# Performance work log

Measured on AMD Instinct MI355X. Metric: run time of the kernel, lower is better.

The kernel has to match this reference:

```python
import jax, jax.numpy as jnp
import numpy as np

B, LATENT = 8192, 1024
NR, NC = 12, 12                      # nb_rows, nb_cols
H0, W0 = NR + 2, NC + 2              # 14x14 after reshape
EPS = 1e-5
SLOPE = 0.01                         # LeakyReLU default


def setup_inputs() -> dict:
    key = jax.random.key(0)
    ks = jax.random.split(key, 9)
    s = 0.05
    return {
        "x": jax.random.normal(ks[0], (B, LATENT), jnp.float32),
        "fc_w": jax.random.normal(ks[1], (H0 * W0 * 36, LATENT), jnp.float32) * s,
        "fc_b": jax.random.normal(ks[2], (H0 * W0 * 36,), jnp.float32) * s,
        "conv_w": jax.random.normal(ks[3], (16, 36, 2, 2), jnp.float32) * s,
        "conv_b": jax.random.normal(ks[4], (16,), jnp.float32) * s,
        "gamma": jnp.ones((16,), jnp.float32),
        "beta": jnp.zeros((16,), jnp.float32),
        # locally-connected weights: (out_ch, in_ch, Hout, Wout, k*k)
        "lw1": jax.random.normal(ks[5], (6, 16, H0 - 1, W0 - 1, 4), jnp.float32) * s,
        "lw2": jax.random.normal(ks[6], (1, 6, H0 - 2, W0 - 2, 4), jnp.float32) * s,
    }


def _leaky(x):
    return jnp.where(x >= 0, x, SLOPE * x)


def _local_conv2(x, w):
    # x: (B,C,H,W); w: (O,C,Ho,Wo,4) with k=2, stride 1, no padding
    Ho, Wo = w.shape[2], w.shape[3]
    patches = jnp.stack(
        [x[:, :, dy:dy + Ho, dx:dx + Wo] for dy in (0, 1) for dx in (0, 1)],
        axis=-1)  # (B,C,Ho,Wo,4)
    return jnp.einsum('bchwk,ochwk->bohw', patches, w)


def reference(x, fc_w, fc_b, conv_w, conv_b, gamma, beta, lw1, lw2):
    # fc -> view(B, H0, W0, 36) -> permute to NCHW
    h = x @ fc_w.T + fc_b
    h = h.reshape(B, H0, W0, 36).transpose(0, 3, 1, 2)  # (B,36,14,14)
    # Conv2d k=2 padding='same' (torch pads bottom/right for even kernels)
    h = jax.lax.conv_general_dilated(
        h, conv_w, window_strides=(1, 1), padding=((0, 1), (0, 1)),
        dimension_numbers=('NCHW', 'OIHW', 'NCHW')) + conv_b[None, :, None, None]
    h = _leaky(h)
    # BatchNorm2d (training mode: batch stats, biased var)
    mu = h.mean(axis=(0, 2, 3), keepdims=True)
    var = h.var(axis=(0, 2, 3), keepdims=True)
    h = (h - mu) * jax.lax.rsqrt(var + EPS)
    h = h * gamma[None, :, None, None] + beta[None, :, None, None]
    # locally-connected stack: 14x14 -> 13x13 -> 12x12
    h = _leaky(_local_conv2(h, lw1))
    return _local_conv2(h, lw2)  # (B,1,12,12)
```

## Files before the change

kernel.cpp:

```cpp
#include <hip/hip_runtime.h>


#define SLOPE 0.01f

typedef __bf16 bf16x8 __attribute__((ext_vector_type(8)));
typedef float f32x4 __attribute__((ext_vector_type(4)));

typedef const __attribute__((address_space(1))) void* gas_ptr;
typedef __attribute__((address_space(3))) void* las_ptr;

__device__ __forceinline__ void load16_to_lds(const void* g, void* l) {
  __builtin_amdgcn_global_load_lds((gas_ptr)g, (las_ptr)l, 16, 0, 0);
}

__device__ __forceinline__ unsigned short f2bf(float f) {
  union { float f; unsigned int u; } v; v.f = f;
  unsigned int r = v.u + 0x7FFFu + ((v.u >> 16) & 1u);
  return (unsigned short)(r >> 16);
}
__device__ __forceinline__ float bfbits2f(unsigned int bits16) {
  union { unsigned int u; float f; } v; v.u = bits16 << 16;
  return v.f;
}
__device__ __forceinline__ float leaky(float v) { return v >= 0.f ? v : SLOPE * v; }

__global__ void k_cast_x(const float* __restrict__ x, unsigned short* __restrict__ xb,
                         float* __restrict__ stats) {
  if (blockIdx.x == 0 && threadIdx.x < 32) stats[threadIdx.x] = 0.f;
  int gid = blockIdx.x * 256 + threadIdx.x;
  const float4* x4 = (const float4*)x;
  float4 a = x4[gid * 2], b = x4[gid * 2 + 1];
  union { unsigned short s[8]; uint4 v; } o;
  o.s[0] = f2bf(a.x); o.s[1] = f2bf(a.y); o.s[2] = f2bf(a.z); o.s[3] = f2bf(a.w);
  o.s[4] = f2bf(b.x); o.s[5] = f2bf(b.y); o.s[6] = f2bf(b.z); o.s[7] = f2bf(b.w);
  ((uint4*)xb)[gid] = o.v;
}

__global__ void k_fold(const float* __restrict__ fc_w, const float* __restrict__ fc_b,
                       const float* __restrict__ conv_w, const float* __restrict__ conv_b,
                       unsigned short* __restrict__ Wc, float* __restrict__ bc) {
  __shared__ float cw[2304];
  int blk = blockIdx.x, kg = blockIdx.y, t = threadIdx.x;
  if (blk == 196) {
    if (kg != 0) return;
    uint4 z = make_uint4(0, 0, 0, 0);
    uint4* dst = (uint4*)(Wc + 3136 * 1024);
    for (int i = t; i < 8192; i += 256) dst[i] = z;
    for (int i = 3136 + t; i < 3200; i += 256) bc[i] = 0.f;
    return;
  }
  for (int i = t; i < 2304; i += 256) cw[i] = conv_w[i];
  __syncthreads();
  int i0 = blk / 14, j0 = blk - (blk / 14) * 14;
  int kcol = kg * 256 + t;
  float acc[16];
#pragma unroll
  for (int o = 0; o < 16; o++) acc[o] = 0.f;
  for (int c = 0; c < 36; c++) {
#pragma unroll
    for (int dy = 0; dy < 2; dy++) {
      int ii = i0 + dy; if (ii > 13) continue;
#pragma unroll
      for (int dx = 0; dx < 2; dx++) {
        int jj = j0 + dx; if (jj > 13) continue;
        int row = (ii * 14 + jj) * 36 + c;
        float f = fc_w[row * 1024 + kcol];
        int kk = dy * 2 + dx;
#pragma unroll
        for (int o = 0; o < 16; o++)
          acc[o] += cw[(o * 36 + c) * 4 + kk] * f;
      }
    }
  }
#pragma unroll
  for (int o = 0; o < 16; o++) {
    int n = o * 196 + i0 * 14 + j0;
    Wc[n * 1024 + kcol] = f2bf(acc[o]);
  }
  if (kg == 0 && t < 16) {
    int o = t;
    float b = conv_b[o];
    for (int c = 0; c < 36; c++)
      for (int dy = 0; dy < 2; dy++) {
        int ii = i0 + dy; if (ii > 13) continue;
        for (int dx = 0; dx < 2; dx++) {
          int jj = j0 + dx; if (jj > 13) continue;
          b += cw[(o * 36 + c) * 4 + dy * 2 + dx] * fc_b[(ii * 14 + jj) * 36 + c];
        }
      }
    bc[o * 196 + i0 * 14 + j0] = b;
  }
}

__global__ __launch_bounds__(256, 4) void k_gemm(const unsigned short* __restrict__ Xb,
                                                 const unsigned short* __restrict__ Wcb,
                                                 const float* __restrict__ bc,
                                                 unsigned short* __restrict__ h2,
                                                 float* __restrict__ stats) {
  __shared__ __align__(16) char lds[32768];
  __shared__ float red[4][4];
  const int t = threadIdx.x;
  const int w = t >> 6, lane = t & 63;
  const int quad = lane >> 4, l15 = lane & 15;
  const int bid = blockIdx.x;
  const int xcd = bid & 7, j = bid >> 3;
  const int mblk = xcd * 8 + (j & 7);
  const int nblk = j >> 3;
  const int m0 = mblk * 128, n0 = nblk * 128;
  const int mrow = t & 127, tko = t >> 7;
  const unsigned short* ga = Xb + (m0 + mrow) * 1024 + tko * 8;
  const unsigned short* gb = Wcb + (n0 + mrow) * 1024 + tko * 8;
  char* lA = lds;
  char* lB = lds + 16384;
  const int wbase = w * 1024;
  const int wm0 = (w >> 1) * 64, wn0 = (w & 1) * 64;

  f32x4 acc[4][4];
#pragma unroll
  for (int a = 0; a < 4; a++)
#pragma unroll
    for (int b = 0; b < 4; b++) acc[a][b] = (f32x4){0.f, 0.f, 0.f, 0.f};

  for (int kb = 0; kb < 1024; kb += 64) {
    __syncthreads();
#pragma unroll
    for (int i = 0; i < 4; i++) {
      load16_to_lds(ga + kb + i * 16, lA + i * 4096 + wbase);
      load16_to_lds(gb + kb + i * 16, lB + i * 4096 + wbase);
    }
    __syncthreads();

#pragma unroll
    for (int kk = 0; kk < 2; kk++) {
      bf16x8 af[4], bfr[4];
#pragma unroll
      for (int mb = 0; mb < 4; mb++)
        af[mb] = *(const bf16x8*)(lA + (kk * 4 + quad) * 2048 + (wm0 + mb * 16 + l15) * 16);
#pragma unroll
      for (int nb = 0; nb < 4; nb++)
        bfr[nb] = *(const bf16x8*)(lB + (kk * 4 + quad) * 2048 + (wn0 + nb * 16 + l15) * 16);
#pragma unroll
      for (int mb = 0; mb < 4; mb++)
#pragma unroll
        for (int nb = 0; nb < 4; nb++)
          acc[mb][nb] = __builtin_amdgcn_mfma_f32_16x16x32_bf16(af[mb], bfr[nb], acc[mb][nb], 0, 0, 0);
    }
  }

  const int cLo = n0 / 196;
  const int cHi = (n0 + 127) / 196;
  float ss0 = 0.f, ss1 = 0.f, sq0 = 0.f, sq1 = 0.f;
#pragma unroll
  for (int nb = 0; nb < 4; nb++) {
    int col = n0 + wn0 + nb * 16 + l15;
    float bias = bc[col];
    int ch = col / 196;
    bool hi = (ch != cLo);
    bool valid = col < 3136;
    float cs = 0.f, cq = 0.f;
#pragma unroll
    for (int mb = 0; mb < 4; mb++) {
#pragma unroll
      for (int r = 0; r < 4; r++) {
        int row = m0 + wm0 + mb * 16 + quad * 4 + r;
        float v = leaky(acc[mb][nb][r] + bias);
        h2[row * 3200 + col] = f2bf(v);
        cs += v; cq += v * v;
      }
    }
    if (valid) {
      if (hi) { ss1 += cs; sq1 += cq; } else { ss0 += cs; sq0 += cq; }
    }
  }
#pragma unroll
  for (int off = 1; off < 64; off <<= 1) {
    ss0 += __shfl_xor(ss0, off, 64);
    ss1 += __shfl_xor(ss1, off, 64);
    sq0 += __shfl_xor(sq0, off, 64);
    sq1 += __shfl_xor(sq1, off, 64);
  }
  if (lane == 0) { red[w][0] = ss0; red[w][1] = ss1; red[w][2] = sq0; red[w][3] = sq1; }
  __syncthreads();
  if (t == 0) {
    float a0 = red[0][0] + red[1][0] + red[2][0] + red[3][0];
    float a1 = red[0][1] + red[1][1] + red[2][1] + red[3][1];
    float b0 = red[0][2] + red[1][2] + red[2][2] + red[3][2];
    float b1 = red[0][3] + red[1][3] + red[2][3] + red[3][3];
    atomicAdd(&stats[cLo], a0);
    atomicAdd(&stats[16 + cLo], b0);
    if (cHi != cLo && cHi < 16) {
      atomicAdd(&stats[cHi], a1);
      atomicAdd(&stats[16 + cHi], b1);
    }
  }
}

__global__ __launch_bounds__(256) void k_tail(const unsigned short* __restrict__ h2,
                                              const float* __restrict__ stats,
                                              const float* __restrict__ gamma,
                                              const float* __restrict__ beta,
                                              const float* __restrict__ lw1,
                                              const float* __restrict__ lw2,
                                              float* __restrict__ out) {
  __shared__ unsigned short h3[4 * 3138];
  __shared__ float h4[4 * 1015];
  __shared__ float sc[16], sh[16];
  int b0 = blockIdx.x * 4, t = threadIdx.x;
  if (t < 16) {
    const float inv = 1.f / 1605632.f;
    float mean = stats[t] * inv;
    float var = stats[16 + t] * inv - mean * mean;
    float rstd = rsqrtf(var + 1e-5f);
    float s = gamma[t] * rstd;
    sc[t] = s; sh[t] = beta[t] - mean * s;
  }
  __syncthreads();
  for (int i = t; i < 6272; i += 256) {
    int bb = i / 1568, q = i - bb * 1568;
    int n = q * 2, o = n / 196;
    unsigned int u = *(const unsigned int*)(h2 + (b0 + bb) * 3200 + n);
    float v0 = bfbits2f(u & 0xffffu) * sc[o] + sh[o];
    float v1 = bfbits2f(u >> 16) * sc[o] + sh[o];
    unsigned int pk = (unsigned int)f2bf(v0) | ((unsigned int)f2bf(v1) << 16);
    *(unsigned int*)(h3 + bb * 3138 + n) = pk;
  }
  __syncthreads();
  for (int u = t; u < 312; u += 256) {
    int bb = u & 3, rest = u >> 2;
    int o = rest / 13, y = rest - o * 13;
    float acc[13];
#pragma unroll
    for (int x = 0; x < 13; x++) acc[x] = 0.f;
    const unsigned short* hb = h3 + bb * 3138;
    for (int c = 0; c < 16; c++) {
      float r0[14], r1[14];
      const unsigned int* p0 = (const unsigned int*)(hb + c * 196 + y * 14);
      const unsigned int* p1 = (const unsigned int*)(hb + c * 196 + (y + 1) * 14);
#pragma unroll
      for (int q = 0; q < 7; q++) {
        unsigned int v0 = p0[q], v1 = p1[q];
        r0[2 * q] = bfbits2f(v0 & 0xffffu); r0[2 * q + 1] = bfbits2f(v0 >> 16);
        r1[2 * q] = bfbits2f(v1 & 0xffffu); r1[2 * q + 1] = bfbits2f(v1 >> 16);
      }
      const float4* wp4 = (const float4*)(lw1 + (((o * 16 + c) * 13 + y) * 13) * 4);
#pragma unroll
      for (int x = 0; x < 13; x++) {
        float4 wv = wp4[x];
        acc[x] += r0[x] * wv.x + r0[x + 1] * wv.y +
                  r1[x] * wv.z + r1[x + 1] * wv.w;
      }
    }
#pragma unroll
    for (int x = 0; x < 13; x++)
      h4[bb * 1015 + (o * 13 + y) * 13 + x] = leaky(acc[x]);
  }
  __syncthreads();
  for (int oi = t; oi < 576; oi += 256) {
    int pos = oi >> 2, bb = oi & 3;
    int y = pos / 12, x = pos - y * 12;
    float a = 0.f;
    const float* hp = h4 + bb * 1015;
    const float4* w4 = (const float4*)lw2;
#pragma unroll
    for (int c = 0; c < 6; c++) {
      float4 wv = w4[(c * 12 + y) * 12 + x];
      int hb = c * 169 + y * 13 + x;
      a += hp[hb] * wv.x + hp[hb + 1] * wv.y +
           hp[hb + 13] * wv.z + hp[hb + 14] * wv.w;
    }
    out[(b0 + bb) * 144 + pos] = a;
  }
}

extern "C" void kernel_launch(void* const* d_in, const int* in_sizes, int n_in,
                              void* d_out, int out_size, void* d_ws, size_t ws_size,
                              hipStream_t stream) {
  const float* x      = (const float*)d_in[0];
  const float* fc_w   = (const float*)d_in[1];
  const float* fc_b   = (const float*)d_in[2];
  const float* conv_w = (const float*)d_in[3];
  const float* conv_b = (const float*)d_in[4];
  const float* gamma  = (const float*)d_in[5];
  const float* beta   = (const float*)d_in[6];
  const float* lw1    = (const float*)d_in[7];
  const float* lw2    = (const float*)d_in[8];

  char* ws = (char*)d_ws;
  unsigned short* Xb    = (unsigned short*)(ws);
  unsigned short* Wc    = (unsigned short*)(ws + 16777216);
  float*          bc    = (float*)(ws + 23330816);
  float*          stats = (float*)(ws + 23343616);
  unsigned short* h2    = (unsigned short*)(ws + 23343744);

  k_cast_x<<<4096, 256, 0, stream>>>(x, Xb, stats);
  k_fold<<<dim3(197, 4), 256, 0, stream>>>(fc_w, fc_b, conv_w, conv_b, Wc, bc);
  k_gemm<<<1600, 256, 0, stream>>>(Xb, Wc, bc, h2, stats);
  k_tail<<<2048, 256, 0, stream>>>(h2, stats, gamma, beta, lw1, lw2, (float*)d_out);
}
```

Baseline: 384.3 us.

## Halve GEMM K-tile to 32 and process two samples per thread in tail kernel

The GEMM kernel now stages a 32-wide K slice per iteration in 16 KB of LDS instead of a 64-wide slice in 32 KB. This lowers LDS use per block, which may allow more resident blocks, but it doubles the number of barrier pairs per K sweep. The tail kernel now handles 8 samples per block instead of 4 and launches half as many blocks. Each thread in the first locally-connected stage computes two samples so every lw1 weight load is reused twice, at the cost of more registers and LDS per block.

```diff
diff --git a/kernel.cpp b/kernel.cpp
--- a/kernel.cpp
+++ b/kernel.cpp
@@ -97,7 +97,7 @@
                                                  const float* __restrict__ bc,
                                                  unsigned short* __restrict__ h2,
                                                  float* __restrict__ stats) {
-  __shared__ __align__(16) char lds[32768];
+  __shared__ __align__(16) char lds[16384];
   __shared__ float red[4][4];
   const int t = threadIdx.x;
   const int w = t >> 6, lane = t & 63;
@@ -111,7 +111,7 @@
   const unsigned short* ga = Xb + (m0 + mrow) * 1024 + tko * 8;
   const unsigned short* gb = Wcb + (n0 + mrow) * 1024 + tko * 8;
   char* lA = lds;
-  char* lB = lds + 16384;
+  char* lB = lds + 8192;
   const int wbase = w * 1024;
   const int wm0 = (w >> 1) * 64, wn0 = (w & 1) * 64;
 
@@ -121,30 +121,26 @@
 #pragma unroll
     for (int b = 0; b < 4; b++) acc[a][b] = (f32x4){0.f, 0.f, 0.f, 0.f};
 
-  for (int kb = 0; kb < 1024; kb += 64) {
+  for (int kb = 0; kb < 1024; kb += 32) {
     __syncthreads();
-#pragma unroll
-    for (int i = 0; i < 4; i++) {
-      load16_to_lds(ga + kb + i * 16, lA + i * 4096 + wbase);
-      load16_to_lds(gb + kb + i * 16, lB + i * 4096 + wbase);
-    }
+    load16_to_lds(ga + kb,      lA + wbase);
+    load16_to_lds(ga + kb + 16, lA + 4096 + wbase);
+    load16_to_lds(gb + kb,      lB + wbase);
+    load16_to_lds(gb + kb + 16, lB + 4096 + wbase);
     __syncthreads();
 
-#pragma unroll
-    for (int kk = 0; kk < 2; kk++) {
-      bf16x8 af[4], bfr[4];
-#pragma unroll
-      for (int mb = 0; mb < 4; mb++)
-        af[mb] = *(const bf16x8*)(lA + (kk * 4 + quad) * 2048 + (wm0 + mb * 16 + l15) * 16);
+    bf16x8 af[4], bfr[4];
+#pragma unroll
+    for (int mb = 0; mb < 4; mb++)
+      af[mb] = *(const bf16x8*)(lA + quad * 2048 + (wm0 + mb * 16 + l15) * 16);
+#pragma unroll
+    for (int nb = 0; nb < 4; nb++)
+      bfr[nb] = *(const bf16x8*)(lB + quad * 2048 + (wn0 + nb * 16 + l15) * 16);
+#pragma unroll
+    for (int mb = 0; mb < 4; mb++)
 #pragma unroll
       for (int nb = 0; nb < 4; nb++)
-        bfr[nb] = *(const bf16x8*)(lB + (kk * 4 + quad) * 2048 + (wn0 + nb * 16 + l15) * 16);
-#pragma unroll
-      for (int mb = 0; mb < 4; mb++)
-#pragma unroll
-        for (int nb = 0; nb < 4; nb++)
-          acc[mb][nb] = __builtin_amdgcn_mfma_f32_16x16x32_bf16(af[mb], bfr[nb], acc[mb][nb], 0, 0, 0);
-    }
+        acc[mb][nb] = __builtin_amdgcn_mfma_f32_16x16x32_bf16(af[mb], bfr[nb], acc[mb][nb], 0, 0, 0);
   }
 
   const int cLo = n0 / 196;
@@ -195,17 +191,17 @@
   }
 }
 
-__global__ __launch_bounds__(256) void k_tail(const unsigned short* __restrict__ h2,
-                                              const float* __restrict__ stats,
-                                              const float* __restrict__ gamma,
-                                              const float* __restrict__ beta,
-                                              const float* __restrict__ lw1,
-                                              const float* __restrict__ lw2,
-                                              float* __restrict__ out) {
-  __shared__ unsigned short h3[4 * 3138];
-  __shared__ float h4[4 * 1015];
+__global__ __launch_bounds__(256, 1) void k_tail(const unsigned short* __restrict__ h2,
+                                                 const float* __restrict__ stats,
+                                                 const float* __restrict__ gamma,
+                                                 const float* __restrict__ beta,
+                                                 const float* __restrict__ lw1,
+                                                 const float* __restrict__ lw2,
+                                                 float* __restrict__ out) {
+  __shared__ unsigned short h3[8 * 3138];
+  __shared__ float h4[8 * 1015];
   __shared__ float sc[16], sh[16];
-  int b0 = blockIdx.x * 4, t = threadIdx.x;
+  int b0 = blockIdx.x * 8, t = threadIdx.x;
   if (t < 16) {
     const float inv = 1.f / 1605632.f;
     float mean = stats[t] * inv;
@@ -215,7 +211,7 @@
     sc[t] = s; sh[t] = beta[t] - mean * s;
   }
   __syncthreads();
-  for (int i = t; i < 6272; i += 256) {
+  for (int i = t; i < 12544; i += 256) {
     int bb = i / 1568, q = i - bb * 1568;
     int n = q * 2, o = n / 196;
     unsigned int u = *(const unsigned int*)(h2 + (b0 + bb) * 3200 + n);
@@ -226,37 +222,45 @@
   }
   __syncthreads();
   for (int u = t; u < 312; u += 256) {
-    int bb = u & 3, rest = u >> 2;
+    int rp = u & 3, rest = u >> 2;
     int o = rest / 13, y = rest - o * 13;
-    float acc[13];
-#pragma unroll
-    for (int x = 0; x < 13; x++) acc[x] = 0.f;
-    const unsigned short* hb = h3 + bb * 3138;
+    int rA = 2 * rp, rB = 2 * rp + 1;
+    float acc0[13], acc1[13];
+#pragma unroll
+    for (int x = 0; x < 13; x++) { acc0[x] = 0.f; acc1[x] = 0.f; }
+    const unsigned short* hA = h3 + rA * 3138;
+    const unsigned short* hB = h3 + rB * 3138;
     for (int c = 0; c < 16; c++) {
-      float r0[14], r1[14];
-      const unsigned int* p0 = (const unsigned int*)(hb + c * 196 + y * 14);
-      const unsigned int* p1 = (const unsigned int*)(hb + c * 196 + (y + 1) * 14);
+      float a0[14], a1[14], b0r[14], b1r[14];
+      const unsigned int* pA0 = (const unsigned int*)(hA + c * 196 + y * 14);
+      const unsigned int* pA1 = (const unsigned int*)(hA + c * 196 + (y + 1) * 14);
+      const unsigned int* pB0 = (const unsigned int*)(hB + c * 196 + y * 14);
+      const unsigned int* pB1 = (const unsigned int*)(hB + c * 196 + (y + 1) * 14);
 #pragma unroll
       for (int q = 0; q < 7; q++) {
-        unsigned int v0 = p0[q], v1 = p1[q];
-        r0[2 * q] = bfbits2f(v0 & 0xffffu); r0[2 * q + 1] = bfbits2f(v0 >> 16);
-        r1[2 * q] = bfbits2f(v1 & 0xffffu); r1[2 * q + 1] = bfbits2f(v1 >> 16);
+        unsigned int vA0 = pA0[q], vA1 = pA1[q], vB0 = pB0[q], vB1 = pB1[q];
+        a0[2 * q] = bfbits2f(vA0 & 0xffffu); a0[2 * q + 1] = bfbits2f(vA0 >> 16);
+        a1[2 * q] = bfbits2f(vA1 & 0xffffu); a1[2 * q + 1] = bfbits2f(vA1 >> 16);
+        b0r[2 * q] = bfbits2f(vB0 & 0xffffu); b0r[2 * q + 1] = bfbits2f(vB0 >> 16);
+        b1r[2 * q] = bfbits2f(vB1 & 0xffffu); b1r[2 * q + 1] = bfbits2f(vB1 >> 16);
       }
       const float4* wp4 = (const float4*)(lw1 + (((o * 16 + c) * 13 + y) * 13) * 4);
 #pragma unroll
       for (int x = 0; x < 13; x++) {
         float4 wv = wp4[x];
-        acc[x] += r0[x] * wv.x + r0[x + 1] * wv.y +
-                  r1[x] * wv.z + r1[x + 1] * wv.w;
-      }
-    }
-#pragma unroll
-    for (int x = 0; x < 13; x++)
-      h4[bb * 1015 + (o * 13 + y) * 13 + x] = leaky(acc[x]);
-  }
-  __syncthreads();
-  for (int oi = t; oi < 576; oi += 256) {
-    int pos = oi >> 2, bb = oi & 3;
+        acc0[x] += a0[x] * wv.x + a0[x + 1] * wv.y + a1[x] * wv.z + a1[x + 1] * wv.w;
+        acc1[x] += b0r[x] * wv.x + b0r[x + 1] * wv.y + b1r[x] * wv.z + b1r[x + 1] * wv.w;
+      }
+    }
+#pragma unroll
+    for (int x = 0; x < 13; x++) {
+      h4[rA * 1015 + (o * 13 + y) * 13 + x] = leaky(acc0[x]);
+      h4[rB * 1015 + (o * 13 + y) * 13 + x] = leaky(acc1[x]);
+    }
+  }
+  __syncthreads();
+  for (int oi = t; oi < 1152; oi += 256) {
+    int pos = oi >> 3, bb = oi & 7;
     int y = pos / 12, x = pos - y * 12;
     float a = 0.f;
     const float* hp = h4 + bb * 1015;
@@ -295,5 +299,5 @@
   k_cast_x<<<4096, 256, 0, stream>>>(x, Xb, stats);
   k_fold<<<dim3(197, 4), 256, 0, stream>>>(fc_w, fc_b, conv_w, conv_b, Wc, bc);
   k_gemm<<<1600, 256, 0, stream>>>(Xb, Wc, bc, h2, stats);
-  k_tail<<<2048, 256, 0, stream>>>(h2, stats, gamma, beta, lw1, lw2, (float*)d_out);
-}
+  k_tail<<<1024, 256, 0, stream>>>(h2, stats, gamma, beta, lw1, lw2, (float*)d_out);
+}
```

New measurement: 419.9 us. 9.2% more time.
